# Kernel optimization log

Measured on AMD Instinct MI355X. Metric: run time of the kernel, lower is better.

The kernel has to match this reference:

```python
import jax, jax.numpy as jnp
import numpy as np

B, S, E, H, ML = 4, 1024, 1024, 16, 2048
HD = E // H


def setup_inputs() -> dict:
    key = jax.random.key(0)
    ks = jax.random.split(key, 8)
    s = 0.02
    return {
        "x": jax.random.normal(ks[0], (B, S, E), dtype=jnp.float32),
        "rel_pos": jax.random.normal(ks[1], (H, ML), dtype=jnp.float32),
        "in_proj_w": jax.random.normal(ks[2], (3 * E, E), dtype=jnp.float32) * s,
        "in_proj_b": jnp.zeros((3 * E,), jnp.float32),
        "out_w": jax.random.normal(ks[3], (E, E), dtype=jnp.float32) * s,
        "out_b": jnp.zeros((E,), jnp.float32),
        "w1": jax.random.normal(ks[4], (4 * E, E), dtype=jnp.float32) * s,
        "b1": jnp.zeros((4 * E,), jnp.float32),
        "w2": jax.random.normal(ks[5], (E, 4 * E), dtype=jnp.float32) * s,
        "b2": jnp.zeros((E,), jnp.float32),
        "ln1_g": jnp.ones((E,), jnp.float32),
        "ln1_b": jnp.zeros((E,), jnp.float32),
        "ln2_g": jnp.ones((E,), jnp.float32),
        "ln2_b": jnp.zeros((E,), jnp.float32),
    }


def _layernorm(x, g, b, eps=1e-5):
    m = x.mean(-1, keepdims=True)
    v = ((x - m) ** 2).mean(-1, keepdims=True)
    return (x - m) * jax.lax.rsqrt(v + eps) * g + b


def _causal_mask(size, rel_pos):
    # rel_pos: [H, max_len]; size <= max_len branch of the torch code
    flipped = jnp.flip(rel_pos[:, :size], -1)                        # [H, size]
    neg_inf = jnp.full((rel_pos.shape[0], size), -jnp.inf, rel_pos.dtype)
    padded = jnp.concatenate([flipped, neg_inf], axis=-1)            # [H, 2*size]
    idx = jnp.arange(size)[None, :] - jnp.arange(size)[:, None] + size - 1
    return padded[:, idx]                                            # [H, S, S]: rel_pos[i-j] if j<=i else -inf


def reference(x, rel_pos, in_proj_w, in_proj_b, out_w, out_b,
              w1, b1, w2, b2, ln1_g, ln1_b, ln2_g, ln2_b):
    b, s, e = x.shape
    xn = _layernorm(x, ln1_g, ln1_b)
    qkv = xn @ in_proj_w.T + in_proj_b                               # [B,S,3E]
    q, k, v = jnp.split(qkv, 3, axis=-1)
    q = q.reshape(b, s, H, HD).transpose(0, 2, 1, 3)                 # [B,H,S,D]
    k = k.reshape(b, s, H, HD).transpose(0, 2, 1, 3)
    v = v.reshape(b, s, H, HD).transpose(0, 2, 1, 3)
    mask = _causal_mask(s, rel_pos)                                  # [H,S,S], broadcast over batch (== repeat(B,1,1))
    scores = jnp.einsum("bhqd,bhkd->bhqk", q, k) / np.sqrt(HD) + mask[None]
    attn = jax.nn.softmax(scores, axis=-1)
    o = jnp.einsum("bhqk,bhkd->bhqd", attn, v)                       # [B,H,S,D]
    o = o.transpose(0, 2, 1, 3).reshape(b, s, e)
    att_out = o @ out_w.T + out_b
    x = x + att_out
    xm = _layernorm(x, ln2_g, ln2_b)
    mlp = jax.nn.relu(xm @ w1.T + b1) @ w2.T + b2
    return x + mlp
```

## Files before the change

### kernel.cpp

```cpp
#include <hip/hip_runtime.h>
#include <stdint.h>

typedef __bf16 bf16x8 __attribute__((ext_vector_type(8)));
typedef float  f32x4  __attribute__((ext_vector_type(4)));

__device__ __forceinline__ unsigned short f2bf(float f) {
  union { float f; unsigned int u; } a; a.f = f;
  unsigned int r = a.u + 0x7FFFu + ((a.u >> 16) & 1u);
  return (unsigned short)(r >> 16);
}

__device__ __forceinline__ unsigned short f2bf_fast(float f) {
  union { __bf16 b; unsigned short u; } v; v.b = (__bf16)f; return v.u;
}

__device__ __forceinline__ void cp16(const void* g, void* l) {
  auto g1 = reinterpret_cast<__attribute__((address_space(1))) unsigned int*>(
      reinterpret_cast<uintptr_t>(g));
  auto l3 = reinterpret_cast<__attribute__((address_space(3))) unsigned int*>(
      reinterpret_cast<uintptr_t>(l));
  __builtin_amdgcn_global_load_lds(g1, l3, 16, 0, 0);
}

__global__ __launch_bounds__(256) void cvt_ln1(
    const float* __restrict__ s0, const float* __restrict__ s1,
    const float* __restrict__ s2, const float* __restrict__ s3,
    unsigned short* __restrict__ d0, unsigned short* __restrict__ d1,
    unsigned short* __restrict__ d2, unsigned short* __restrict__ d3,
    const float* __restrict__ x,
    const float* __restrict__ g,
    const float* __restrict__ bta,
    unsigned short* __restrict__ out,
    const float* __restrict__ seed_bias,
    float* __restrict__ seed_out) {
  if (blockIdx.x < 12288) {
    int i = (blockIdx.x * 256 + threadIdx.x) * 4;
    const float* src; unsigned short* dst; int off;
    if (i < 3145728)       { src = s0; dst = d0; off = 0; }
    else if (i < 4194304)  { src = s1; dst = d1; off = 3145728; }
    else if (i < 8388608)  { src = s2; dst = d2; off = 4194304; }
    else                   { src = s3; dst = d3; off = 8388608; }
    i -= off;
    float4 v = *(const float4*)(src + i);
    union { unsigned short u[4]; uint2 p; } o;
    o.u[0] = f2bf(v.x); o.u[1] = f2bf(v.y); o.u[2] = f2bf(v.z); o.u[3] = f2bf(v.w);
    *(uint2*)(dst + i) = o.p;
    return;
  }
  const int row = blockIdx.x - 12288, t = threadIdx.x;
  const float4 v = *(const float4*)(x + (size_t)row * 1024 + t * 4);
  {
    float4 sb = *(const float4*)(seed_bias + t * 4);
    float4 sv;
    sv.x = v.x + sb.x; sv.y = v.y + sb.y; sv.z = v.z + sb.z; sv.w = v.w + sb.w;
    *(float4*)(seed_out + (size_t)row * 1024 + t * 4) = sv;
  }
  float s1v = v.x + v.y + v.z + v.w;
  float s2v = v.x*v.x + v.y*v.y + v.z*v.z + v.w*v.w;
  #pragma unroll
  for (int off = 1; off < 64; off <<= 1) {
    s1v += __shfl_xor(s1v, off, 64);
    s2v += __shfl_xor(s2v, off, 64);
  }
  __shared__ float r1[4], r2[4];
  if ((t & 63) == 0) { r1[t >> 6] = s1v; r2[t >> 6] = s2v; }
  __syncthreads();
  s1v = r1[0] + r1[1] + r1[2] + r1[3];
  s2v = r2[0] + r2[1] + r2[2] + r2[3];
  const float mean = s1v * (1.0f / 1024.0f);
  const float var  = s2v * (1.0f / 1024.0f) - mean * mean;
  const float rstd = rsqrtf(var + 1e-5f);
  const float4 gv = *(const float4*)(g + t * 4);
  const float4 bv = *(const float4*)(bta + t * 4);
  union { unsigned short u[4]; uint2 p; } o;
  o.u[0] = f2bf((v.x - mean) * rstd * gv.x + bv.x);
  o.u[1] = f2bf((v.y - mean) * rstd * gv.y + bv.y);
  o.u[2] = f2bf((v.z - mean) * rstd * gv.z + bv.z);
  o.u[3] = f2bf((v.w - mean) * rstd * gv.w + bv.w);
  *(uint2*)(out + (size_t)row * 1024 + t * 4) = o.p;
}

__global__ __launch_bounds__(256) void ln_bf16_seed(
    const float* __restrict__ x,
    const float* __restrict__ g,
    const float* __restrict__ bta,
    unsigned short* __restrict__ out,
    const float* __restrict__ seed_bias,
    float* __restrict__ seed_out) {
  const int row = blockIdx.x, t = threadIdx.x;
  const float4 v = *(const float4*)(x + (size_t)row * 1024 + t * 4);
  {
    float4 sb = *(const float4*)(seed_bias + t * 4);
    float4 sv;
    sv.x = v.x + sb.x; sv.y = v.y + sb.y; sv.z = v.z + sb.z; sv.w = v.w + sb.w;
    *(float4*)(seed_out + (size_t)row * 1024 + t * 4) = sv;
  }
  float s1 = v.x + v.y + v.z + v.w;
  float s2 = v.x*v.x + v.y*v.y + v.z*v.z + v.w*v.w;
  #pragma unroll
  for (int off = 1; off < 64; off <<= 1) {
    s1 += __shfl_xor(s1, off, 64);
    s2 += __shfl_xor(s2, off, 64);
  }
  __shared__ float r1[4], r2[4];
  if ((t & 63) == 0) { r1[t >> 6] = s1; r2[t >> 6] = s2; }
  __syncthreads();
  s1 = r1[0] + r1[1] + r1[2] + r1[3];
  s2 = r2[0] + r2[1] + r2[2] + r2[3];
  const float mean = s1 * (1.0f / 1024.0f);
  const float var  = s2 * (1.0f / 1024.0f) - mean * mean;
  const float rstd = rsqrtf(var + 1e-5f);
  const float4 gv = *(const float4*)(g + t * 4);
  const float4 bv = *(const float4*)(bta + t * 4);
  union { unsigned short u[4]; uint2 p; } o;
  o.u[0] = f2bf((v.x - mean) * rstd * gv.x + bv.x);
  o.u[1] = f2bf((v.y - mean) * rstd * gv.y + bv.y);
  o.u[2] = f2bf((v.z - mean) * rstd * gv.z + bv.z);
  o.u[3] = f2bf((v.w - mean) * rstd * gv.w + bv.w);
  *(uint2*)(out + (size_t)row * 1024 + t * 4) = o.p;
}

template <int MODE>
__device__ __forceinline__ void gemm_core(
    const unsigned short* __restrict__ A,
    const unsigned short* __restrict__ Bt,
    const float* __restrict__ bias,
    void* __restrict__ outp,
    int N, int K, int kbeg, int kend,
    unsigned short* As, unsigned short* Bs) {
  const int tid = threadIdx.x;
  const int wave = tid >> 6, lane = tid & 63;
  const int q = lane >> 4, c = lane & 15;
  const int wm = (wave & 1) << 6, wn = (wave >> 1) << 6;
  const int m0 = blockIdx.x << 7, n0 = blockIdx.y << 7;

  const int srow = tid >> 3;
  const int cg8  = ((tid & 7) ^ (srow & 7)) << 3;

  const unsigned short* gA = A  + (size_t)(m0 + srow) * K + cg8;
  const unsigned short* gB = Bt + (size_t)(n0 + srow) * K + cg8;
  const size_t rstep = (size_t)32 * K;

  auto issue = [&](int k0, int buf) {
    unsigned short* lA = As + buf * 8192 + tid * 8;
    unsigned short* lB = Bs + buf * 8192 + tid * 8;
    #pragma unroll
    for (int it = 0; it < 4; it++) {
      cp16(gA + it * rstep + k0, lA + it * 2048);
      cp16(gB + it * rstep + k0, lB + it * 2048);
    }
  };

  const f32x4 fzero = {0.f, 0.f, 0.f, 0.f};
  f32x4 acc[4][4];
  #pragma unroll
  for (int i = 0; i < 4; i++)
    #pragma unroll
    for (int j = 0; j < 4; j++) acc[i][j] = fzero;

  issue(kbeg, 0);
  if (kbeg + 64 < kend) issue(kbeg + 64, 1);

  int buf = 0;
  for (int k0 = kbeg; k0 < kend; k0 += 64, buf ^= 1) {
    if (k0 + 64 < kend) asm volatile("s_waitcnt vmcnt(8)" ::: "memory");
    else                asm volatile("s_waitcnt vmcnt(0)" ::: "memory");
    asm volatile("s_barrier" ::: "memory");

    const unsigned short* cA = As + buf * 8192;
    const unsigned short* cB = Bs + buf * 8192;
    #pragma unroll
    for (int ks = 0; ks < 2; ks++) {
      const int sw = (((ks << 2) + q) ^ (c & 7)) << 3;
      bf16x8 af[4], bf[4];
      #pragma unroll
      for (int i = 0; i < 4; i++) af[i] = *(const bf16x8*)&cA[(wm + i*16 + c)*64 + sw];
      #pragma unroll
      for (int j = 0; j < 4; j++) bf[j] = *(const bf16x8*)&cB[(wn + j*16 + c)*64 + sw];
      #pragma unroll
      for (int i = 0; i < 4; i++)
        #pragma unroll
        for (int j = 0; j < 4; j++)
          acc[i][j] = __builtin_amdgcn_mfma_f32_16x16x32_bf16(af[i], bf[j], acc[i][j], 0, 0, 0);
    }

    asm volatile("s_barrier" ::: "memory");
    if (k0 + 128 < kend) issue(k0 + 128, buf);
  }

  if (MODE == 4) {
    float* op = (float*)outp;
    #pragma unroll
    for (int i = 0; i < 4; i++) {
      #pragma unroll
      for (int r = 0; r < 4; r++) {
        const int row = m0 + wm + i * 16 + q * 4 + r;
        #pragma unroll
        for (int j = 0; j < 4; j++) {
          const int col = n0 + wn + j * 16 + c;
          atomicAdd(op + (size_t)row * N + col, acc[i][j][r]);
        }
      }
    }
  } else {
    float bj[4];
    #pragma unroll
    for (int j = 0; j < 4; j++) bj[j] = bias[n0 + wn + j * 16 + c];
    #pragma unroll
    for (int i = 0; i < 4; i++) {
      #pragma unroll
      for (int r = 0; r < 4; r++) {
        const int row = m0 + wm + i * 16 + q * 4 + r;
        #pragma unroll
        for (int j = 0; j < 4; j++) {
          const int col = n0 + wn + j * 16 + c;
          const size_t idx = (size_t)row * N + col;
          float v = acc[i][j][r] + bj[j];
          if (MODE == 0) ((unsigned short*)outp)[idx] = f2bf(v);
          else           ((unsigned short*)outp)[idx] = f2bf(fmaxf(v, 0.f));
        }
      }
    }
  }
}

template <int MODE>
__global__ __launch_bounds__(256, 2) void gemm_bt(
    const unsigned short* __restrict__ A,
    const unsigned short* __restrict__ Bt,
    const float* __restrict__ bias,
    void* __restrict__ outp,
    int N, int K) {
  __shared__ __align__(16) unsigned short As[2 * 8192];
  __shared__ __align__(16) unsigned short Bs[2 * 8192];
  gemm_core<MODE>(A, Bt, bias, outp, N, K, 0, K, As, Bs);
}

__global__ __launch_bounds__(256, 2) void gemm_bt_splitk(
    const unsigned short* __restrict__ A,
    const unsigned short* __restrict__ Bt,
    float* __restrict__ outp,
    int N, int K) {
  __shared__ __align__(16) unsigned short As[2 * 8192];
  __shared__ __align__(16) unsigned short Bs[2 * 8192];
  const int KH = K >> 1;
  const int kbeg = blockIdx.z * KH;
  gemm_core<4>(A, Bt, nullptr, outp, N, K, kbeg, kbeg + KH, As, Bs);
}

__global__ __launch_bounds__(256, 2) void attn_flash(
    const unsigned short* __restrict__ qkv,
    const float* __restrict__ rel_pos,
    unsigned short* __restrict__ o) {
  __shared__ __align__(16) unsigned short Qs[128 * 64];
  __shared__ __align__(16) unsigned short Ks[64 * 64];
  __shared__ __align__(16) unsigned short Vs[64 * 64];
  __shared__ __align__(16) unsigned short Ps[4][32 * 64];
  __shared__ float rps[1024];

  const int tid = threadIdx.x;
  const int wave = tid >> 6, lane = tid & 63;
  const int q = lane >> 4, c = lane & 15;

  const int lid = blockIdx.x + (blockIdx.y << 3);
  const int xq = lid & 7, y = lid >> 3;
  const int qt = (y & 32) ? (7 - xq) : xq;
  const int b = y >> 4, h = y & 15;

  const unsigned short* qg = qkv + (size_t)b * 1024 * 3072 + h * 64;
  const unsigned short* kg = qg + 1024;
  const unsigned short* vg = qg + 2048;

  #pragma unroll
  for (int i = 0; i < 4; i++) {
    const int idx = tid + i * 256;
    rps[idx & 1023] = rel_pos[h * 2048 + (idx & 1023)] * 1.44269504f;
  }

  const int sr  = tid >> 3;
  const int cg8 = ((tid & 7) ^ (sr & 7)) << 3;
  #pragma unroll
  for (int it = 0; it < 4; it++)
    cp16(qg + (size_t)(qt * 128 + sr + it * 32) * 3072 + cg8, &Qs[(tid + it * 256) * 8]);
  __syncthreads();

  bf16x8 qf[2][2];
  #pragma unroll
  for (int mt = 0; mt < 2; mt++)
    #pragma unroll
    for (int ks = 0; ks < 2; ks++)
      qf[mt][ks] = *(const bf16x8*)&Qs[(wave*32 + mt*16 + c)*64 + ((((ks<<2)+q) ^ (c & 7)) << 3)];

  const f32x4 fzero = {0.f, 0.f, 0.f, 0.f};
  f32x4 O[2][4];
  float l_i[2][4];
  #pragma unroll
  for (int mt = 0; mt < 2; mt++) {
    #pragma unroll
    for (int r = 0; r < 4; r++) l_i[mt][r] = 0.f;
    #pragma unroll
    for (int dt = 0; dt < 4; dt++) O[mt][dt] = fzero;
  }

  unsigned short* Pw = &Ps[wave][0];
  const int i_base = qt * 128 + wave * 32;
  const int vrow = tid & 63, d0 = (tid >> 6) << 4;
  const int vchunk = vrow >> 3, vlo = vrow & 7;

  const float sc = 0.125f * 1.44269504f;
  const int kdiag = qt << 1;
  const int nkt = (qt + 1) * 2;

  for (int kt = 0; kt < nkt; kt++) {
    __syncthreads();
    cp16(kg + (size_t)(kt * 64 + sr) * 3072 + cg8, &Ks[tid * 8]);
    cp16(kg + (size_t)(kt * 64 + sr + 32) * 3072 + cg8, &Ks[(tid + 256) * 8]);
    {
      union { int4 v; unsigned short u[8]; } va, vb2;
      const unsigned short* vrp = vg + (size_t)(kt * 64 + vrow) * 3072 + d0;
      va.v  = *(const int4*)vrp;
      vb2.v = *(const int4*)(vrp + 8);
      #pragma unroll
      for (int j = 0; j < 8; j++) {
        const int pos = ((vchunk ^ j) << 3) + vlo;
        Vs[(d0 + j) * 64 + pos]     = va.u[j];
        Vs[(d0 + 8 + j) * 64 + pos] = vb2.u[j];
      }
    }
    __syncthreads();

    f32x4 S[2][4];
    #pragma unroll
    for (int mt = 0; mt < 2; mt++)
      #pragma unroll
      for (int nt = 0; nt < 4; nt++) S[mt][nt] = fzero;
    #pragma unroll
    for (int ks = 0; ks < 2; ks++) {
      const int sw = (((ks << 2) + q) ^ (c & 7)) << 3;
      bf16x8 kb[4];
      #pragma unroll
      for (int nt = 0; nt < 4; nt++) kb[nt] = *(const bf16x8*)&Ks[(nt*16 + c)*64 + sw];
      #pragma unroll
      for (int mt = 0; mt < 2; mt++)
        #pragma unroll
        for (int nt = 0; nt < 4; nt++)
          S[mt][nt] = __builtin_amdgcn_mfma_f32_16x16x32_bf16(qf[mt][ks], kb[nt], S[mt][nt], 0, 0, 0);
    }

    if (kt < kdiag) {
      #pragma unroll
      for (int mt = 0; mt < 2; mt++) {
        #pragma unroll
        for (int r = 0; r < 4; r++) {
          const int i_ = i_base + mt * 16 + q * 4 + r;
          const int prow = (mt * 16 + q * 4 + r) * 64;
          const int rsw  = (q * 4 + r) & 7;
          float s = 0.f;
          #pragma unroll
          for (int nt = 0; nt < 4; nt++) {
            const int j_ = kt * 64 + nt * 16 + c;
            const float p = exp2f(fmaf(S[mt][nt][r], sc, rps[i_ - j_]));
            s += p;
            Pw[prow + ((((nt << 1) + (c >> 3)) ^ rsw) << 3) + (c & 7)] = f2bf_fast(p);
          }
          l_i[mt][r] += s;
        }
      }
    } else {
      #pragma unroll
      for (int mt = 0; mt < 2; mt++) {
        #pragma unroll
        for (int r = 0; r < 4; r++) {
          const int i_ = i_base + mt * 16 + q * 4 + r;
          const int prow = (mt * 16 + q * 4 + r) * 64;
          const int rsw  = (q * 4 + r) & 7;
          float s = 0.f;
          #pragma unroll
          for (int nt = 0; nt < 4; nt++) {
            const int j_ = kt * 64 + nt * 16 + c;
            const int d_ = i_ - j_;
            const float p = (d_ >= 0)
                ? exp2f(fmaf(S[mt][nt][r], sc, rps[d_ & 1023])) : 0.f;
            s += p;
            Pw[prow + ((((nt << 1) + (c >> 3)) ^ rsw) << 3) + (c & 7)] = f2bf_fast(p);
          }
          l_i[mt][r] += s;
        }
      }
    }

    asm volatile("s_waitcnt lgkmcnt(0)" ::: "memory");

    #pragma unroll
    for (int ks = 0; ks < 2; ks++) {
      const int sw = (((ks << 2) + q) ^ (c & 7)) << 3;
      bf16x8 pa[2], vb[4];
      #pragma unroll
      for (int mt = 0; mt < 2; mt++) pa[mt] = *(const bf16x8*)&Pw[(mt*16 + c)*64 + sw];
      #pragma unroll
      for (int dt = 0; dt < 4; dt++) vb[dt] = *(const bf16x8*)&Vs[(dt*16 + c)*64 + sw];
      #pragma unroll
      for (int mt = 0; mt < 2; mt++)
        #pragma unroll
        for (int dt = 0; dt < 4; dt++)
          O[mt][dt] = __builtin_amdgcn_mfma_f32_16x16x32_bf16(pa[mt], vb[dt], O[mt][dt], 0, 0, 0);
    }
  }

  #pragma unroll
  for (int mt = 0; mt < 2; mt++) {
    #pragma unroll
    for (int r = 0; r < 4; r++) {
      float l = l_i[mt][r];
      l += __shfl_xor(l, 1, 64);
      l += __shfl_xor(l, 2, 64);
      l += __shfl_xor(l, 4, 64);
      l += __shfl_xor(l, 8, 64);
      const float inv = 1.0f / l;
      const int i_ = i_base + mt * 16 + q * 4 + r;
      unsigned short* orow = o + (size_t)(b * 1024 + i_) * 1024 + h * 64 + c;
      #pragma unroll
      for (int dt = 0; dt < 4; dt++) orow[dt * 16] = f2bf(O[mt][dt][r] * inv);
    }
  }
}

extern "C" void kernel_launch(void* const* d_in, const int* in_sizes, int n_in,
                              void* d_out, int out_size, void* d_ws, size_t ws_size,
                              hipStream_t stream) {
  (void)in_sizes; (void)n_in; (void)out_size; (void)ws_size;
  const float* x    = (const float*)d_in[0];
  const float* rel  = (const float*)d_in[1];
  const float* ipw  = (const float*)d_in[2];
  const float* ipb  = (const float*)d_in[3];
  const float* outw = (const float*)d_in[4];
  const float* outb = (const float*)d_in[5];
  const float* w1   = (const float*)d_in[6];
  const float* b1   = (const float*)d_in[7];
  const float* w2   = (const float*)d_in[8];
  const float* b2   = (const float*)d_in[9];
  const float* ln1g = (const float*)d_in[10];
  const float* ln1b = (const float*)d_in[11];
  const float* ln2g = (const float*)d_in[12];
  const float* ln2b = (const float*)d_in[13];

  unsigned short* ipw_b  = (unsigned short*)d_ws;
  unsigned short* outw_b = ipw_b  + (size_t)3072 * 1024;
  unsigned short* w1_b   = outw_b + (size_t)1024 * 1024;
  unsigned short* w2_b   = w1_b   + (size_t)4096 * 1024;
  unsigned short* xn     = w2_b   + (size_t)1024 * 4096;
  unsigned short* qkvb   = xn     + (size_t)4096 * 1024;
  unsigned short* ob     = qkvb   + (size_t)4096 * 3072;
  unsigned short* hb     = qkvb;
  unsigned short* xm     = xn;
  float*          x2     = (float*)(ob + (size_t)4096 * 1024);

  cvt_ln1<<<16384, 256, 0, stream>>>(ipw, outw, w1, w2, ipw_b, outw_b, w1_b, w2_b,
                                     x, ln1g, ln1b, xn, outb, x2);

  gemm_bt<0><<<dim3(32, 24), 256, 0, stream>>>(xn, ipw_b, ipb, qkvb, 3072, 1024);

  attn_flash<<<dim3(8, 64), 256, 0, stream>>>(qkvb, rel, ob);

  gemm_bt_splitk<<<dim3(32, 8, 2), 256, 0, stream>>>(ob, outw_b, x2, 1024, 1024);

  ln_bf16_seed<<<4096, 256, 0, stream>>>(x2, ln2g, ln2b, xm, b2, (float*)d_out);

  gemm_bt<2><<<dim3(32, 32), 256, 0, stream>>>(xm, w1_b, b1, hb, 4096, 1024);

  gemm_bt_splitk<<<dim3(32, 8, 2), 256, 0, stream>>>(hb, w2_b, (float*)d_out, 1024, 4096);
}
```

Measured before the change: 327.9 us.

## Add 256x256-tile 8-wave GEMM with interleaved staging for QKV and FC1

Adds a new bf16 MFMA GEMM kernel that uses 256x256 output tiles, 512 threads and double-buffered LDS. Each K-step is split into four quarter-tile compute phases, with global-to-LDS loads for the next tiles interleaved between them, plus workgroup swizzling and s_setprio around the MFMA blocks. The QKV projection and the first MLP GEMM now use it instead of the 128-tile gemm_bt. The aim is more data reuse per tile and better overlap of loads with math. In exchange there are fewer workgroups (192 and 256), which may underfill 256 CUs, and register pressure is higher.

```diff
diff --git a/kernel.cpp b/kernel.cpp
--- a/kernel.cpp
+++ b/kernel.cpp
@@ -248,6 +248,174 @@
   gemm_core<4>(A, Bt, nullptr, outp, N, K, kbeg, kbeg + KH, As, Bs);
 }
 
+template <int MODE>
+__global__ __launch_bounds__(512, 2) void gemm256(
+    const unsigned short* __restrict__ A,
+    const unsigned short* __restrict__ Bt,
+    const float* __restrict__ bias,
+    unsigned short* __restrict__ outp,
+    int N, int K, int nbn) {
+  __shared__ __align__(16) unsigned short As[2][2][8192];
+  __shared__ __align__(16) unsigned short Bs[2][2][8192];
+
+  const int tid = threadIdx.x;
+  const int wave = tid >> 6, lane = tid & 63;
+  const int q = lane >> 4, c = lane & 15;
+  const int wm = wave >> 2;
+  const int wn = wave & 3;
+  const int bh = wn >> 1;
+  const int bcol0 = (wn & 1) << 6;
+
+  const int nwg = gridDim.x;
+  const int bid = blockIdx.x;
+  const int swz = (bid & 7) * (nwg >> 3) + (bid >> 3);
+  const int m0 = (swz / nbn) << 8, n0 = (swz % nbn) << 8;
+
+  const int NT = K >> 6;
+
+  const int srow = tid >> 3;
+  const int cg8  = ((tid & 7) ^ (srow & 7)) << 3;
+
+  const unsigned short* gA = A  + (size_t)(m0 + srow) * K + cg8;
+  const unsigned short* gB = Bt + (size_t)(n0 + srow) * K + cg8;
+  const size_t rstep64  = (size_t)64 * K;
+  const size_t rstep128 = (size_t)128 * K;
+
+  auto stage = [&](int t, int h) {
+    const int buf = t & 1;
+    const int k0 = t << 6;
+    if (h < 2) {
+      unsigned short* l = &As[buf][h][0] + tid * 8;
+      const unsigned short* gp = gA + (size_t)h * rstep128 + k0;
+      cp16(gp, l);
+      cp16(gp + rstep64, l + 4096);
+    } else {
+      unsigned short* l = &Bs[buf][h - 2][0] + tid * 8;
+      const unsigned short* gp = gB + (size_t)(h - 2) * rstep128 + k0;
+      cp16(gp, l);
+      cp16(gp + rstep64, l + 4096);
+    }
+  };
+
+  const f32x4 fzero = {0.f, 0.f, 0.f, 0.f};
+  f32x4 acc[8][4];
+  #pragma unroll
+  for (int i = 0; i < 8; i++)
+    #pragma unroll
+    for (int j = 0; j < 4; j++) acc[i][j] = fzero;
+
+  stage(0, 0); stage(0, 1); stage(0, 2); stage(0, 3);
+  if (NT > 1) {
+    stage(1, 0); stage(1, 1);
+    asm volatile("s_waitcnt vmcnt(4)" ::: "memory");
+  } else {
+    asm volatile("s_waitcnt vmcnt(0)" ::: "memory");
+  }
+  asm volatile("s_barrier" ::: "memory");
+
+  for (int t = 0; t < NT; ++t) {
+    const int buf = t & 1;
+    const unsigned short* cA = &As[buf][wm][0];
+    const unsigned short* cB = &Bs[buf][bh][0];
+
+    bf16x8 a[8][2], b[4][2];
+
+    #pragma unroll
+    for (int i = 0; i < 4; i++)
+      #pragma unroll
+      for (int ks = 0; ks < 2; ks++)
+        a[i][ks] = *(const bf16x8*)&cA[(i*16 + c)*64 + ((((ks<<2)+q) ^ (c & 7)) << 3)];
+    #pragma unroll
+    for (int j = 0; j < 2; j++)
+      #pragma unroll
+      for (int ks = 0; ks < 2; ks++)
+        b[j][ks] = *(const bf16x8*)&cB[(bcol0 + j*16 + c)*64 + ((((ks<<2)+q) ^ (c & 7)) << 3)];
+    if (t + 1 < NT) stage(t + 1, 2);
+    asm volatile("s_barrier" ::: "memory");
+    asm volatile("s_waitcnt lgkmcnt(0)" ::: "memory");
+    __builtin_amdgcn_s_setprio(1);
+    #pragma unroll
+    for (int i = 0; i < 4; i++)
+      #pragma unroll
+      for (int j = 0; j < 2; j++)
+        #pragma unroll
+        for (int ks = 0; ks < 2; ks++)
+          acc[i][j] = __builtin_amdgcn_mfma_f32_16x16x32_bf16(a[i][ks], b[j][ks], acc[i][j], 0, 0, 0);
+    __builtin_amdgcn_s_setprio(0);
+    asm volatile("s_barrier" ::: "memory");
+
+    #pragma unroll
+    for (int i = 4; i < 8; i++)
+      #pragma unroll
+      for (int ks = 0; ks < 2; ks++)
+        a[i][ks] = *(const bf16x8*)&cA[(i*16 + c)*64 + ((((ks<<2)+q) ^ (c & 7)) << 3)];
+    #pragma unroll
+    for (int j = 2; j < 4; j++)
+      #pragma unroll
+      for (int ks = 0; ks < 2; ks++)
+        b[j][ks] = *(const bf16x8*)&cB[(bcol0 + j*16 + c)*64 + ((((ks<<2)+q) ^ (c & 7)) << 3)];
+    if (t + 1 < NT) stage(t + 1, 3);
+    asm volatile("s_barrier" ::: "memory");
+    asm volatile("s_waitcnt lgkmcnt(0)" ::: "memory");
+    __builtin_amdgcn_s_setprio(1);
+    #pragma unroll
+    for (int i = 4; i < 8; i++)
+      #pragma unroll
+      for (int j = 2; j < 4; j++)
+        #pragma unroll
+        for (int ks = 0; ks < 2; ks++)
+          acc[i][j] = __builtin_amdgcn_mfma_f32_16x16x32_bf16(a[i][ks], b[j][ks], acc[i][j], 0, 0, 0);
+    __builtin_amdgcn_s_setprio(0);
+    asm volatile("s_barrier" ::: "memory");
+
+    if (t + 2 < NT) stage(t + 2, 0);
+    asm volatile("s_barrier" ::: "memory");
+    __builtin_amdgcn_s_setprio(1);
+    #pragma unroll
+    for (int i = 0; i < 4; i++)
+      #pragma unroll
+      for (int j = 2; j < 4; j++)
+        #pragma unroll
+        for (int ks = 0; ks < 2; ks++)
+          acc[i][j] = __builtin_amdgcn_mfma_f32_16x16x32_bf16(a[i][ks], b[j][ks], acc[i][j], 0, 0, 0);
+    __builtin_amdgcn_s_setprio(0);
+    asm volatile("s_barrier" ::: "memory");
+
+    if (t + 2 < NT) stage(t + 2, 1);
+    asm volatile("s_barrier" ::: "memory");
+    __builtin_amdgcn_s_setprio(1);
+    #pragma unroll
+    for (int i = 4; i < 8; i++)
+      #pragma unroll
+      for (int j = 0; j < 2; j++)
+        #pragma unroll
+        for (int ks = 0; ks < 2; ks++)
+          acc[i][j] = __builtin_amdgcn_mfma_f32_16x16x32_bf16(a[i][ks], b[j][ks], acc[i][j], 0, 0, 0);
+    __builtin_amdgcn_s_setprio(0);
+    if (t + 2 < NT)      asm volatile("s_waitcnt vmcnt(4)" ::: "memory");
+    else if (t + 1 < NT) asm volatile("s_waitcnt vmcnt(0)" ::: "memory");
+    if (t + 1 < NT) asm volatile("s_barrier" ::: "memory");
+  }
+
+  float bj[4];
+  #pragma unroll
+  for (int j = 0; j < 4; j++) bj[j] = bias[n0 + wn * 64 + j * 16 + c];
+  #pragma unroll
+  for (int i = 0; i < 8; i++) {
+    const int row = m0 + wm * 128 + i * 16 + q * 4;
+    #pragma unroll
+    for (int rr = 0; rr < 4; rr++) {
+      unsigned short* orow = outp + (size_t)(row + rr) * N + n0 + wn * 64 + c;
+      #pragma unroll
+      for (int j = 0; j < 4; j++) {
+        float v = acc[i][j][rr] + bj[j];
+        if (MODE == 2) v = fmaxf(v, 0.f);
+        orow[j * 16] = f2bf(v);
+      }
+    }
+  }
+}
+
 __global__ __launch_bounds__(256, 2) void attn_flash(
     const unsigned short* __restrict__ qkv,
     const float* __restrict__ rel_pos,
@@ -458,7 +626,7 @@
   cvt_ln1<<<16384, 256, 0, stream>>>(ipw, outw, w1, w2, ipw_b, outw_b, w1_b, w2_b,
                                      x, ln1g, ln1b, xn, outb, x2);
 
-  gemm_bt<0><<<dim3(32, 24), 256, 0, stream>>>(xn, ipw_b, ipb, qkvb, 3072, 1024);
+  gemm256<0><<<192, 512, 0, stream>>>(xn, ipw_b, ipb, qkvb, 3072, 1024, 12);
 
   attn_flash<<<dim3(8, 64), 256, 0, stream>>>(qkvb, rel, ob);
 
@@ -466,7 +634,7 @@
 
   ln_bf16_seed<<<4096, 256, 0, stream>>>(x2, ln2g, ln2b, xm, b2, (float*)d_out);
 
-  gemm_bt<2><<<dim3(32, 32), 256, 0, stream>>>(xm, w1_b, b1, hb, 4096, 1024);
+  gemm256<2><<<256, 512, 0, stream>>>(xm, w1_b, b1, hb, 4096, 1024, 16);
 
   gemm_bt_splitk<<<dim3(32, 8, 2), 256, 0, stream>>>(hb, w2_b, (float*)d_out, 1024, 4096);
 }
```

After: 335.8 us. 1.02x slower.

## Triple-buffer A tiles in GEMM core to prefetch A one step further ahead

Applied to the files above, without the earlier changes.

The GEMM main loop now keeps three LDS buffers for the A tile and two for the B tile. A loads are issued three k-steps ahead and B loads two steps ahead, with graduated vmcnt waits. The goal is to hide more global-load latency for the A operand. It costs an extra 16KB of LDS per block (64KB total), which could limit occupancy under the 2-blocks launch bound.

```diff
diff --git a/kernel.cpp b/kernel.cpp
--- a/kernel.cpp
+++ b/kernel.cpp
@@ -141,14 +141,15 @@
   const unsigned short* gB = Bt + (size_t)(n0 + srow) * K + cg8;
   const size_t rstep = (size_t)32 * K;
 
-  auto issue = [&](int k0, int buf) {
+  auto issueA = [&](int k0, int buf) {
     unsigned short* lA = As + buf * 8192 + tid * 8;
+    #pragma unroll
+    for (int it = 0; it < 4; it++) cp16(gA + it * rstep + k0, lA + it * 2048);
+  };
+  auto issueB = [&](int k0, int buf) {
     unsigned short* lB = Bs + buf * 8192 + tid * 8;
     #pragma unroll
-    for (int it = 0; it < 4; it++) {
-      cp16(gA + it * rstep + k0, lA + it * 2048);
-      cp16(gB + it * rstep + k0, lB + it * 2048);
-    }
+    for (int it = 0; it < 4; it++) cp16(gB + it * rstep + k0, lB + it * 2048);
   };
 
   const f32x4 fzero = {0.f, 0.f, 0.f, 0.f};
@@ -158,17 +159,21 @@
     #pragma unroll
     for (int j = 0; j < 4; j++) acc[i][j] = fzero;
 
-  issue(kbeg, 0);
-  if (kbeg + 64 < kend) issue(kbeg + 64, 1);
-
-  int buf = 0;
-  for (int k0 = kbeg; k0 < kend; k0 += 64, buf ^= 1) {
-    if (k0 + 64 < kend) asm volatile("s_waitcnt vmcnt(8)" ::: "memory");
-    else                asm volatile("s_waitcnt vmcnt(0)" ::: "memory");
+  const int NT = (kend - kbeg) >> 6;
+
+  issueA(kbeg, 0); issueB(kbeg, 0);
+  if (NT > 1) { issueA(kbeg + 64, 1); issueB(kbeg + 64, 1); }
+  if (NT > 2) issueA(kbeg + 128, 2);
+
+  int ba = 0, bb = 0;
+  for (int t = 0; t < NT; ++t) {
+    if (t + 2 < NT)      asm volatile("s_waitcnt vmcnt(12)" ::: "memory");
+    else if (t + 1 < NT) asm volatile("s_waitcnt vmcnt(8)" ::: "memory");
+    else                 asm volatile("s_waitcnt vmcnt(0)" ::: "memory");
     asm volatile("s_barrier" ::: "memory");
 
-    const unsigned short* cA = As + buf * 8192;
-    const unsigned short* cB = Bs + buf * 8192;
+    const unsigned short* cA = As + ba * 8192;
+    const unsigned short* cB = Bs + bb * 8192;
     #pragma unroll
     for (int ks = 0; ks < 2; ks++) {
       const int sw = (((ks << 2) + q) ^ (c & 7)) << 3;
@@ -185,7 +190,10 @@
     }
 
     asm volatile("s_barrier" ::: "memory");
-    if (k0 + 128 < kend) issue(k0 + 128, buf);
+    if (t + 2 < NT) issueB(kbeg + (t + 2) * 64, bb);
+    if (t + 3 < NT) issueA(kbeg + (t + 3) * 64, ba);
+    ba = (ba == 2) ? 0 : ba + 1;
+    bb ^= 1;
   }
 
   if (MODE == 4) {
@@ -231,7 +239,7 @@
     const float* __restrict__ bias,
     void* __restrict__ outp,
     int N, int K) {
-  __shared__ __align__(16) unsigned short As[2 * 8192];
+  __shared__ __align__(16) unsigned short As[3 * 8192];
   __shared__ __align__(16) unsigned short Bs[2 * 8192];
   gemm_core<MODE>(A, Bt, bias, outp, N, K, 0, K, As, Bs);
 }
@@ -241,7 +249,7 @@
     const unsigned short* __restrict__ Bt,
     float* __restrict__ outp,
     int N, int K) {
-  __shared__ __align__(16) unsigned short As[2 * 8192];
+  __shared__ __align__(16) unsigned short As[3 * 8192];
   __shared__ __align__(16) unsigned short Bs[2 * 8192];
   const int KH = K >> 1;
   const int kbeg = blockIdx.z * KH;
```

New measurement: 334.3 us. About the same (+1.9%).
